# Kernel tuning notes

Hardware: AMD Instinct MI355X
Metric: run time of the kernel (lower is better)

Reference implementation:

```python
import jax, jax.numpy as jnp
import numpy as np


def _dct_last(x):
    """Unnormalized DCT-II along the last axis via the FFT reorder+twiddle trick:
    v[n] = x[2n], v[N-1-n] = x[2n+1];  y[k] = Re( exp(-i*pi*k/(2N)) * FFT(v)[k] )
    => y[k] = sum_n x[n] * cos(pi*(2n+1)*k/(2N))
    This mirrors DREAMPlace's expk (twiddle) formulation.
    """
    N = x.shape[-1]
    v = jnp.concatenate([x[..., ::2], x[..., 1::2][..., ::-1]], axis=-1)
    V = jnp.fft.fft(v)
    k = jnp.arange(N)
    expk = jnp.exp(-1j * jnp.pi * k.astype(x.dtype) / (2.0 * N))
    return jnp.real(V * expk).astype(x.dtype)


def _dct2(x):
    # DCT-II along last axis, then along second-to-last axis (separable 2D DCT).
    y = _dct_last(x)
    y = _dct_last(jnp.swapaxes(y, -1, -2))
    return jnp.swapaxes(y, -1, -2)


def setup_inputs() -> dict:
    key = jax.random.key(0)
    x = jax.random.normal(key, (8, 2048, 2048), dtype=jnp.float32)
    return {"x": x}


def reference(x):
    return _dct2(x)
```

## Files before the change

### kernel.cpp

```cpp
#include <hip/hip_runtime.h>
#include <hip/hip_bf16.h>
#include <hip/hip_fp16.h>


typedef _Float16 half8 __attribute__((ext_vector_type(8)));
typedef float f32x4 __attribute__((ext_vector_type(4)));
typedef unsigned int uint32;

constexpr int BK = 32;
constexpr int BM = 256, BN = 256;
constexpr int KK = 1024;
constexpr int NT = KK / BK;
constexpr int TILE_E = BM * BK;

__device__ __forceinline__ unsigned short f2h_bits(float f) {
  _Float16 h = (_Float16)f;
  return __builtin_bit_cast(unsigned short, h);
}

__device__ __forceinline__ void gload_lds16(const unsigned short* g, unsigned short* l) {
  __builtin_amdgcn_global_load_lds((const __attribute__((address_space(1))) void*)g,
                                   (__attribute__((address_space(3))) void*)l,
                                   16, 0, 0);
}

#define CFENCE asm volatile("" ::: "memory")

__device__ __forceinline__ int swz_idx(int r, int cbyte) {
  int b = (r >> 1) * 128 + ((((r & 1) << 6) | cbyte) ^ (((r >> 1) & 7) << 4));
  return b >> 1;
}

__device__ __forceinline__ void stage_tile(const unsigned short* __restrict__ G,
                                           int rowbase, int k0, int ld,
                                           unsigned short* lds, int wave, int lane) {
#pragma unroll
  for (int c = 0; c < 2; ++c) {
    const int p = c * 64 + wave * 8 + (lane >> 3);
    const int v = (lane & 7) ^ ((lane >> 3) & 7);
    const int r = 2 * p + (v >> 2);
    const int kslot = v & 3;
    const unsigned short* src = G + (size_t)(rowbase + r) * ld + (k0 + kslot * 8);
    unsigned short* dst = lds + (c * 64 + wave * 8) * 64;
    gload_lds16(src, dst);
  }
}

__global__ __launch_bounds__(256) void cvt_fold12(const float* __restrict__ x,
                                                  unsigned short* __restrict__ Xff) {
  int tid = blockIdx.x * 256 + threadIdx.x;
  int m = tid >> 7;
  int b = m >> 10;
  int ui = m & 1023;
  int j0 = (tid & 127) << 3;
  const float* rf = x + ((size_t)b * 2048 + ui) * 2048;
  const float* rb = x + ((size_t)b * 2048 + 2047 - ui) * 2048;
  float4 fa = *(const float4*)(rf + j0);
  float4 fb = *(const float4*)(rf + j0 + 4);
  float4 fc = *(const float4*)(rf + 2040 - j0);
  float4 fd = *(const float4*)(rf + 2044 - j0);
  float4 ga = *(const float4*)(rb + j0);
  float4 gb = *(const float4*)(rb + j0 + 4);
  float4 gc = *(const float4*)(rb + 2040 - j0);
  float4 gd = *(const float4*)(rb + 2044 - j0);
  float f[8] = {fa.x, fa.y, fa.z, fa.w, fb.x, fb.y, fb.z, fb.w};
  float fm[8] = {fd.w, fd.z, fd.y, fd.x, fc.w, fc.z, fc.y, fc.x};
  float g[8] = {ga.x, ga.y, ga.z, ga.w, gb.x, gb.y, gb.z, gb.w};
  float gm[8] = {gd.w, gd.z, gd.y, gd.x, gc.w, gc.z, gc.y, gc.x};
  uint32 ss[4], sd[4], ds[4], dd[4];
#pragma unroll
  for (int e = 0; e < 4; ++e) {
#pragma unroll
    for (int h = 0; h < 2; ++h) {
      int k = 2 * e + h;
      float fs = f[k] + fm[k], fdv = f[k] - fm[k];
      float gs = g[k] + gm[k], gdv = g[k] - gm[k];
      uint32 vss = f2h_bits(fs + gs), vsd = f2h_bits(fdv + gdv);
      uint32 vds = f2h_bits(fs - gs), vdd = f2h_bits(fdv - gdv);
      if (h == 0) { ss[e] = vss; sd[e] = vsd; ds[e] = vds; dd[e] = vdd; }
      else { ss[e] |= vss << 16; sd[e] |= vsd << 16; ds[e] |= vds << 16; dd[e] |= vdd << 16; }
    }
  }
  unsigned short* os = Xff + ((size_t)b * 2048 + ui) * 2048 + j0;
  unsigned short* od = Xff + ((size_t)b * 2048 + 1024 + ui) * 2048 + j0;
  *(uint4*)os = make_uint4(ss[0], ss[1], ss[2], ss[3]);
  *(uint4*)(os + 1024) = make_uint4(sd[0], sd[1], sd[2], sd[3]);
  *(uint4*)od = make_uint4(ds[0], ds[1], ds[2], ds[3]);
  *(uint4*)(od + 1024) = make_uint4(dd[0], dd[1], dd[2], dd[3]);
}

__global__ __launch_bounds__(256) void gen_cos2(unsigned short* __restrict__ Ce,
                                                unsigned short* __restrict__ Co) {
  int idx = blockIdx.x * 256 + threadIdx.x;
  int k = idx >> 10, n = idx & 1023;
  int tn = 2 * n + 1;
  int pe = (tn * (2 * k)) & 8191;
  int po = (tn * (2 * k + 1)) & 8191;
  const float s = 7.6699039394282061e-4f;
  Ce[idx] = f2h_bits(cosf((float)pe * s));
  Co[idx] = f2h_bits(cosf((float)po * s));
}

template <int MODE>
__global__ __launch_bounds__(512) void dct_gemm(
    const unsigned short* __restrict__ Ce, const unsigned short* __restrict__ Co,
    const unsigned short* __restrict__ D, void* __restrict__ outp) {
  __shared__ unsigned short As[4 * TILE_E];
  __shared__ unsigned short Bs[4 * TILE_E];

  const int tid = threadIdx.x;
  const int lane = tid & 63;
  const int wave = tid >> 6;
  const int wr = wave >> 2;
  const int wc = wave & 3;
  const int bm = blockIdx.y * BM;
  const int bn = blockIdx.x * BN;
  const int z = blockIdx.z;

  const unsigned short* Ag;
  const unsigned short* Bg;
  int lda, ldb, arow, brow;
  bool half;
  if (MODE == 0) {
    half = (bn >= 1024);
    Ag = D + (half ? 1024 : 0); lda = 2048; arow = bm;
    Bg = half ? Co : Ce;        ldb = 1024; brow = bn - (half ? 1024 : 0);
  } else {
    half = (bm >= 1024);
    Ag = half ? Co : Ce;        lda = 1024; arow = bm - (half ? 1024 : 0);
    Bg = D + (size_t)z * 4194304u + (half ? 1024 : 0);
    ldb = 2048; brow = bn;
  }

  const int frc = lane & 15;
  const int cb = (lane >> 4) << 4;

  f32x4 acc[8][4] = {};

  stage_tile(Ag, arow, 0, lda, &As[0], wave, lane);
  stage_tile(Bg, brow, 0, ldb, &Bs[0], wave, lane);
  stage_tile(Ag, arow, BK, lda, &As[TILE_E], wave, lane);
  stage_tile(Bg, brow, BK, ldb, &Bs[TILE_E], wave, lane);
  asm volatile("s_waitcnt vmcnt(4)" ::: "memory");
  CFENCE; __builtin_amdgcn_s_barrier(); CFENCE;

  for (int t = 0; t < NT; ++t) {
    const unsigned short* at = &As[(t & 3) * TILE_E];
    const unsigned short* bt = &Bs[(t & 3) * TILE_E];
    half8 af[4], bf[4];

#pragma unroll
    for (int m = 0; m < 4; ++m)
      af[m] = *(const half8*)&at[swz_idx(wr * 128 + m * 16 + frc, cb)];
#pragma unroll
    for (int n = 0; n < 4; ++n)
      bf[n] = *(const half8*)&bt[swz_idx(wc * 64 + n * 16 + frc, cb)];
    if (t + 2 < NT)
      stage_tile(Ag, arow, (t + 2) * BK, lda, &As[((t + 2) & 3) * TILE_E], wave, lane);
    CFENCE; __builtin_amdgcn_s_barrier(); CFENCE;
    __builtin_amdgcn_s_setprio(1);
#pragma unroll
    for (int m = 0; m < 4; ++m)
#pragma unroll
      for (int n = 0; n < 4; ++n)
        acc[m][n] = __builtin_amdgcn_mfma_f32_16x16x32_f16(af[m], bf[n], acc[m][n], 0, 0, 0);
    __builtin_amdgcn_s_setprio(0);

#pragma unroll
    for (int m = 0; m < 4; ++m)
      af[m] = *(const half8*)&at[swz_idx(wr * 128 + 64 + m * 16 + frc, cb)];
    if (t + 2 < NT)
      stage_tile(Bg, brow, (t + 2) * BK, ldb, &Bs[((t + 2) & 3) * TILE_E], wave, lane);
    if (t < NT - 2)
      asm volatile("s_waitcnt vmcnt(4)" ::: "memory");
    else if (t == NT - 2)
      asm volatile("s_waitcnt vmcnt(0)" ::: "memory");
    CFENCE; __builtin_amdgcn_s_barrier(); CFENCE;
    __builtin_amdgcn_s_setprio(1);
#pragma unroll
    for (int m = 0; m < 4; ++m)
#pragma unroll
      for (int n = 0; n < 4; ++n)
        acc[m + 4][n] =
            __builtin_amdgcn_mfma_f32_16x16x32_f16(af[m], bf[n], acc[m + 4][n], 0, 0, 0);
    __builtin_amdgcn_s_setprio(0);
  }

  const int koff = half ? 1024 : 0;
  if (MODE == 0) {
    unsigned short* U2t = (unsigned short*)outp;
#pragma unroll
    for (int mi = 0; mi < 8; ++mi) {
      const int r = bm + wr * 128 + (mi >> 2) * 64 + (mi & 3) * 16 + (lane >> 4) * 4;
      const int b = r >> 11;
      const int rb = r & 2047;
#pragma unroll
      for (int n = 0; n < 4; ++n) {
        const int cpk = bn + wc * 64 + n * 16 + frc;
        const int ktrue = 2 * (cpk - koff) + (half ? 1 : 0);
        uint32 lo = f2h_bits(acc[mi][n][0]) | ((uint32)f2h_bits(acc[mi][n][1]) << 16);
        uint32 hi = f2h_bits(acc[mi][n][2]) | ((uint32)f2h_bits(acc[mi][n][3]) << 16);
        *(uint2*)&U2t[(size_t)b * 4194304 + (size_t)ktrue * 2048 + rb] =
            make_uint2(lo, hi);
      }
    }
  } else {
    float* out = (float*)outp + (size_t)z * 4194304;
#pragma unroll
    for (int mi = 0; mi < 8; ++mi) {
      const int p0 =
          bm + wr * 128 + (mi >> 2) * 64 + (mi & 3) * 16 + (lane >> 4) * 4 - koff;
#pragma unroll
      for (int n = 0; n < 4; ++n) {
        const int cg = bn + wc * 64 + n * 16 + frc;
#pragma unroll
        for (int i = 0; i < 4; ++i) {
          const int rtrue = 2 * (p0 + i) + (half ? 1 : 0);
          out[(size_t)rtrue * 2048 + cg] = acc[mi][n][i];
        }
      }
    }
  }
}

extern "C" void kernel_launch(void* const* d_in, const int* in_sizes, int n_in,
                              void* d_out, int out_size, void* d_ws,
                              size_t ws_size, hipStream_t stream) {
  const float* x = (const float*)d_in[0];
  float* out = (float*)d_out;

  unsigned short* Xff = (unsigned short*)d_ws;
  unsigned short* Ce = Xff + 33554432u;
  unsigned short* Co = Ce + 1048576u;
  unsigned short* U2t = Co + 1048576u;

  cvt_fold12<<<4096, 256, 0, stream>>>(x, Xff);
  gen_cos2<<<4096, 256, 0, stream>>>(Ce, Co);
  dct_gemm<0><<<dim3(8, 64, 1), 512, 0, stream>>>(Ce, Co, Xff, (void*)U2t);
  dct_gemm<1><<<dim3(8, 8, 8), 512, 0, stream>>>(Ce, Co, U2t, (void*)out);
}
```

Measured before the change: 208.5 us.

## Apply second-level even/odd DCT fold to shrink even-index GEMM depth

The even-frequency half of each 1D DCT is folded once more into 4k and 4k+2 classes. A new fused conversion kernel builds four-way butterflies over rows and columns, and a new table generator emits three cosine matrices. Each GEMM stage now runs as two launches: one with K=1024 for the odd outputs and one with K=512 for the two even sub-classes. This cuts total MFMA work by about a quarter. In exchange it adds an extra launch per stage, short K loops whose pipeline prologue and epilogue are proportionally larger, and more complex index mapping in the fold kernel.

Result: no change. 207.0 us (-0.7%).

```diff
diff --git a/kernel.cpp b/kernel.cpp
--- a/kernel.cpp
+++ b/kernel.cpp
@@ -7,11 +7,7 @@
 typedef float f32x4 __attribute__((ext_vector_type(4)));
 typedef unsigned int uint32;
 
-constexpr int BK = 32;
-constexpr int BM = 256, BN = 256;
-constexpr int KK = 1024;
-constexpr int NT = KK / BK;
-constexpr int TILE_E = BM * BK;
+constexpr int TILE_E = 256 * 32;
 
 __device__ __forceinline__ unsigned short f2h_bits(float f) {
   _Float16 h = (_Float16)f;
@@ -46,65 +42,107 @@
   }
 }
 
-__global__ __launch_bounds__(256) void cvt_fold12(const float* __restrict__ x,
+__global__ __launch_bounds__(256) void cvt_fold22(const float* __restrict__ x,
                                                   unsigned short* __restrict__ Xff) {
   int tid = blockIdx.x * 256 + threadIdx.x;
-  int m = tid >> 7;
-  int b = m >> 10;
-  int ui = m & 1023;
-  int j0 = (tid & 127) << 3;
-  const float* rf = x + ((size_t)b * 2048 + ui) * 2048;
-  const float* rb = x + ((size_t)b * 2048 + 2047 - ui) * 2048;
-  float4 fa = *(const float4*)(rf + j0);
-  float4 fb = *(const float4*)(rf + j0 + 4);
-  float4 fc = *(const float4*)(rf + 2040 - j0);
-  float4 fd = *(const float4*)(rf + 2044 - j0);
-  float4 ga = *(const float4*)(rb + j0);
-  float4 gb = *(const float4*)(rb + j0 + 4);
-  float4 gc = *(const float4*)(rb + 2040 - j0);
-  float4 gd = *(const float4*)(rb + 2044 - j0);
-  float f[8] = {fa.x, fa.y, fa.z, fa.w, fb.x, fb.y, fb.z, fb.w};
-  float fm[8] = {fd.w, fd.z, fd.y, fd.x, fc.w, fc.z, fc.y, fc.x};
-  float g[8] = {ga.x, ga.y, ga.z, ga.w, gb.x, gb.y, gb.z, gb.w};
-  float gm[8] = {gd.w, gd.z, gd.y, gd.x, gc.w, gc.z, gc.y, gc.x};
-  uint32 ss[4], sd[4], ds[4], dd[4];
-#pragma unroll
-  for (int e = 0; e < 4; ++e) {
-#pragma unroll
-    for (int h = 0; h < 2; ++h) {
-      int k = 2 * e + h;
-      float fs = f[k] + fm[k], fdv = f[k] - fm[k];
-      float gs = g[k] + gm[k], gdv = g[k] - gm[k];
-      uint32 vss = f2h_bits(fs + gs), vsd = f2h_bits(fdv + gdv);
-      uint32 vds = f2h_bits(fs - gs), vdd = f2h_bits(fdv - gdv);
-      if (h == 0) { ss[e] = vss; sd[e] = vsd; ds[e] = vds; dd[e] = vdd; }
-      else { ss[e] |= vss << 16; sd[e] |= vsd << 16; ds[e] |= vds << 16; dd[e] |= vdd << 16; }
-    }
-  }
-  unsigned short* os = Xff + ((size_t)b * 2048 + ui) * 2048 + j0;
-  unsigned short* od = Xff + ((size_t)b * 2048 + 1024 + ui) * 2048 + j0;
-  *(uint4*)os = make_uint4(ss[0], ss[1], ss[2], ss[3]);
-  *(uint4*)(os + 1024) = make_uint4(sd[0], sd[1], sd[2], sd[3]);
-  *(uint4*)od = make_uint4(ds[0], ds[1], ds[2], ds[3]);
-  *(uint4*)(od + 1024) = make_uint4(dd[0], dd[1], dd[2], dd[3]);
-}
-
-__global__ __launch_bounds__(256) void gen_cos2(unsigned short* __restrict__ Ce,
-                                                unsigned short* __restrict__ Co) {
+  int m = tid >> 6;
+  int b = m >> 9;
+  int v = m & 511;
+  int j0 = (tid & 63) << 3;
+  const float* base = x + (size_t)b * 4194304;
+  const float* rows[4] = {base + (size_t)v * 2048, base + (size_t)(2047 - v) * 2048,
+                          base + (size_t)(1023 - v) * 2048, base + (size_t)(1024 + v) * 2048};
+  unsigned short* o[4] = {
+      Xff + ((size_t)b * 2048 + v) * 2048,
+      Xff + ((size_t)b * 2048 + 512 + v) * 2048,
+      Xff + ((size_t)b * 2048 + 1024 + v) * 2048,
+      Xff + ((size_t)b * 2048 + 2047 - v) * 2048};
+
+#pragma unroll
+  for (int h = 0; h < 2; ++h) {
+    const int ja = j0 + h * 4;
+    const int jb = 1020 - j0 - h * 4;
+    const int jc = 1024 + j0 + h * 4;
+    const int jd = 2044 - j0 - h * 4;
+    float4 va[4], vb[4], vc[4], vd[4];
+#pragma unroll
+    for (int t = 0; t < 4; ++t) {
+      va[t] = *(const float4*)(rows[t] + ja);
+      vb[t] = *(const float4*)(rows[t] + jb);
+      vc[t] = *(const float4*)(rows[t] + jc);
+      vd[t] = *(const float4*)(rows[t] + jd);
+    }
+    unsigned short up[4][4], um[4][4], wn[4][4], wm[4][4];
+#pragma unroll
+    for (int e4 = 0; e4 < 4; ++e4) {
+      float A[4], Bq[4], C[4], Dq[4];
+#pragma unroll
+      for (int t = 0; t < 4; ++t) {
+        A[t] = ((const float*)&va[t])[e4];
+        Bq[t] = ((const float*)&vb[t])[3 - e4];
+        C[t] = ((const float*)&vc[t])[e4];
+        Dq[t] = ((const float*)&vd[t])[3 - e4];
+      }
+      float Av[4] = {A[0] + A[1] + A[2] + A[3], A[0] + A[1] - A[2] - A[3],
+                     A[0] - A[1], A[2] - A[3]};
+      float Bv[4] = {Bq[0] + Bq[1] + Bq[2] + Bq[3], Bq[0] + Bq[1] - Bq[2] - Bq[3],
+                     Bq[0] - Bq[1], Bq[2] - Bq[3]};
+      float Cv[4] = {C[0] + C[1] + C[2] + C[3], C[0] + C[1] - C[2] - C[3],
+                     C[0] - C[1], C[2] - C[3]};
+      float Dv[4] = {Dq[0] + Dq[1] + Dq[2] + Dq[3], Dq[0] + Dq[1] - Dq[2] - Dq[3],
+                     Dq[0] - Dq[1], Dq[2] - Dq[3]};
+#pragma unroll
+      for (int t = 0; t < 4; ++t) {
+        float un = Av[t] + Dv[t];
+        float umr = Bv[t] + Cv[t];
+        up[t][e4] = f2h_bits(un + umr);
+        um[t][e4] = f2h_bits(un - umr);
+        wn[t][e4] = f2h_bits(Av[t] - Dv[t]);
+        wm[t][e4] = f2h_bits(Bv[t] - Cv[t]);
+      }
+    }
+#pragma unroll
+    for (int t = 0; t < 4; ++t) {
+      *(uint2*)(o[t] + ja) =
+          make_uint2(up[t][0] | ((uint32)up[t][1] << 16), up[t][2] | ((uint32)up[t][3] << 16));
+      *(uint2*)(o[t] + 512 + ja) =
+          make_uint2(um[t][0] | ((uint32)um[t][1] << 16), um[t][2] | ((uint32)um[t][3] << 16));
+      *(uint2*)(o[t] + 1024 + ja) =
+          make_uint2(wn[t][0] | ((uint32)wn[t][1] << 16), wn[t][2] | ((uint32)wn[t][3] << 16));
+      *(uint2*)(o[t] + 1024 + jb) =
+          make_uint2(wm[t][3] | ((uint32)wm[t][2] << 16), wm[t][1] | ((uint32)wm[t][0] << 16));
+    }
+  }
+}
+
+__global__ __launch_bounds__(256) void gen_cos3(unsigned short* __restrict__ C4k,
+                                                unsigned short* __restrict__ C2h,
+                                                unsigned short* __restrict__ C4h) {
   int idx = blockIdx.x * 256 + threadIdx.x;
-  int k = idx >> 10, n = idx & 1023;
-  int tn = 2 * n + 1;
-  int pe = (tn * (2 * k)) & 8191;
-  int po = (tn * (2 * k + 1)) & 8191;
   const float s = 7.6699039394282061e-4f;
-  Ce[idx] = f2h_bits(cosf((float)pe * s));
-  Co[idx] = f2h_bits(cosf((float)po * s));
-}
-
-template <int MODE>
+  if (idx < 1048576) {
+    int k = idx >> 10, n = idx & 1023;
+    int t = ((2 * n + 1) * (2 * k + 1)) & 8191;
+    C4k[idx] = f2h_bits(cosf((float)t * s));
+  } else if (idx < 1310720) {
+    int i2 = idx - 1048576;
+    int k = i2 >> 9, n = i2 & 511;
+    int t = ((2 * n + 1) * 4 * k) & 8191;
+    C2h[i2] = f2h_bits(cosf((float)t * s));
+  } else {
+    int i2 = idx - 1310720;
+    int k = i2 >> 9, n = i2 & 511;
+    int t = ((2 * n + 1) * (4 * k + 2)) & 8191;
+    C4h[i2] = f2h_bits(cosf((float)t * s));
+  }
+}
+
+template <int MODE, int SPLIT>
 __global__ __launch_bounds__(512) void dct_gemm(
-    const unsigned short* __restrict__ Ce, const unsigned short* __restrict__ Co,
+    const unsigned short* __restrict__ M0, const unsigned short* __restrict__ M1,
     const unsigned short* __restrict__ D, void* __restrict__ outp) {
+  constexpr int K = SPLIT ? 512 : 1024;
+  constexpr int NT = K / 32;
   __shared__ unsigned short As[4 * TILE_E];
   __shared__ unsigned short Bs[4 * TILE_E];
 
@@ -113,23 +151,29 @@
   const int wave = tid >> 6;
   const int wr = wave >> 2;
   const int wc = wave & 3;
-  const int bm = blockIdx.y * BM;
-  const int bn = blockIdx.x * BN;
+  const int bmx = blockIdx.y;
+  const int bnx = blockIdx.x;
   const int z = blockIdx.z;
 
   const unsigned short* Ag;
   const unsigned short* Bg;
-  int lda, ldb, arow, brow;
-  bool half;
+  int lda, ldb, arow, brow, cls;
   if (MODE == 0) {
-    half = (bn >= 1024);
-    Ag = D + (half ? 1024 : 0); lda = 2048; arow = bm;
-    Bg = half ? Co : Ce;        ldb = 1024; brow = bn - (half ? 1024 : 0);
+    cls = SPLIT ? (bnx >> 1) : 0;
+    Ag = D + (SPLIT ? cls * 512 : 1024);
+    lda = 2048;
+    arow = bmx * 256;
+    Bg = SPLIT ? (cls ? M1 : M0) : M0;
+    ldb = K;
+    brow = (SPLIT ? (bnx & 1) : bnx) * 256;
   } else {
-    half = (bm >= 1024);
-    Ag = half ? Co : Ce;        lda = 1024; arow = bm - (half ? 1024 : 0);
-    Bg = D + (size_t)z * 4194304u + (half ? 1024 : 0);
-    ldb = 2048; brow = bn;
+    cls = SPLIT ? (bmx >> 1) : 0;
+    Ag = SPLIT ? (cls ? M1 : M0) : M0;
+    lda = K;
+    arow = (SPLIT ? (bmx & 1) : bmx) * 256;
+    Bg = D + (size_t)z * 4194304u + (SPLIT ? cls * 512 : 1024);
+    ldb = 2048;
+    brow = bnx * 256;
   }
 
   const int frc = lane & 15;
@@ -139,8 +183,8 @@
 
   stage_tile(Ag, arow, 0, lda, &As[0], wave, lane);
   stage_tile(Bg, brow, 0, ldb, &Bs[0], wave, lane);
-  stage_tile(Ag, arow, BK, lda, &As[TILE_E], wave, lane);
-  stage_tile(Bg, brow, BK, ldb, &Bs[TILE_E], wave, lane);
+  stage_tile(Ag, arow, 32, lda, &As[TILE_E], wave, lane);
+  stage_tile(Bg, brow, 32, ldb, &Bs[TILE_E], wave, lane);
   asm volatile("s_waitcnt vmcnt(4)" ::: "memory");
   CFENCE; __builtin_amdgcn_s_barrier(); CFENCE;
 
@@ -156,7 +200,7 @@
     for (int n = 0; n < 4; ++n)
       bf[n] = *(const half8*)&bt[swz_idx(wc * 64 + n * 16 + frc, cb)];
     if (t + 2 < NT)
-      stage_tile(Ag, arow, (t + 2) * BK, lda, &As[((t + 2) & 3) * TILE_E], wave, lane);
+      stage_tile(Ag, arow, (t + 2) * 32, lda, &As[((t + 2) & 3) * TILE_E], wave, lane);
     CFENCE; __builtin_amdgcn_s_barrier(); CFENCE;
     __builtin_amdgcn_s_setprio(1);
 #pragma unroll
@@ -170,7 +214,7 @@
     for (int m = 0; m < 4; ++m)
       af[m] = *(const half8*)&at[swz_idx(wr * 128 + 64 + m * 16 + frc, cb)];
     if (t + 2 < NT)
-      stage_tile(Bg, brow, (t + 2) * BK, ldb, &Bs[((t + 2) & 3) * TILE_E], wave, lane);
+      stage_tile(Bg, brow, (t + 2) * 32, ldb, &Bs[((t + 2) & 3) * TILE_E], wave, lane);
     if (t < NT - 2)
       asm volatile("s_waitcnt vmcnt(4)" ::: "memory");
     else if (t == NT - 2)
@@ -186,18 +230,17 @@
     __builtin_amdgcn_s_setprio(0);
   }
 
-  const int koff = half ? 1024 : 0;
   if (MODE == 0) {
     unsigned short* U2t = (unsigned short*)outp;
 #pragma unroll
     for (int mi = 0; mi < 8; ++mi) {
-      const int r = bm + wr * 128 + (mi >> 2) * 64 + (mi & 3) * 16 + (lane >> 4) * 4;
+      const int r = arow + wr * 128 + (mi >> 2) * 64 + (mi & 3) * 16 + (lane >> 4) * 4;
       const int b = r >> 11;
       const int rb = r & 2047;
 #pragma unroll
       for (int n = 0; n < 4; ++n) {
-        const int cpk = bn + wc * 64 + n * 16 + frc;
-        const int ktrue = 2 * (cpk - koff) + (half ? 1 : 0);
+        const int ccls = brow + wc * 64 + n * 16 + frc;
+        const int ktrue = SPLIT ? (4 * ccls + 2 * cls) : (2 * ccls + 1);
         uint32 lo = f2h_bits(acc[mi][n][0]) | ((uint32)f2h_bits(acc[mi][n][1]) << 16);
         uint32 hi = f2h_bits(acc[mi][n][2]) | ((uint32)f2h_bits(acc[mi][n][3]) << 16);
         *(uint2*)&U2t[(size_t)b * 4194304 + (size_t)ktrue * 2048 + rb] =
@@ -208,14 +251,13 @@
     float* out = (float*)outp + (size_t)z * 4194304;
 #pragma unroll
     for (int mi = 0; mi < 8; ++mi) {
-      const int p0 =
-          bm + wr * 128 + (mi >> 2) * 64 + (mi & 3) * 16 + (lane >> 4) * 4 - koff;
+      const int p0 = arow + wr * 128 + (mi >> 2) * 64 + (mi & 3) * 16 + (lane >> 4) * 4;
 #pragma unroll
       for (int n = 0; n < 4; ++n) {
-        const int cg = bn + wc * 64 + n * 16 + frc;
+        const int cg = brow + wc * 64 + n * 16 + frc;
 #pragma unroll
         for (int i = 0; i < 4; ++i) {
-          const int rtrue = 2 * (p0 + i) + (half ? 1 : 0);
+          const int rtrue = SPLIT ? (4 * (p0 + i) + 2 * cls) : (2 * (p0 + i) + 1);
           out[(size_t)rtrue * 2048 + cg] = acc[mi][n][i];
         }
       }
@@ -230,12 +272,15 @@
   float* out = (float*)d_out;
 
   unsigned short* Xff = (unsigned short*)d_ws;
-  unsigned short* Ce = Xff + 33554432u;
-  unsigned short* Co = Ce + 1048576u;
-  unsigned short* U2t = Co + 1048576u;
-
-  cvt_fold12<<<4096, 256, 0, stream>>>(x, Xff);
-  gen_cos2<<<4096, 256, 0, stream>>>(Ce, Co);
-  dct_gemm<0><<<dim3(8, 64, 1), 512, 0, stream>>>(Ce, Co, Xff, (void*)U2t);
-  dct_gemm<1><<<dim3(8, 8, 8), 512, 0, stream>>>(Ce, Co, U2t, (void*)out);
-}
+  unsigned short* C4k = Xff + 33554432u;
+  unsigned short* C2h = C4k + 1048576u;
+  unsigned short* C4h = C2h + 262144u;
+  unsigned short* U2t = C4h + 262144u;
+
+  cvt_fold22<<<1024, 256, 0, stream>>>(x, Xff);
+  gen_cos3<<<6144, 256, 0, stream>>>(C4k, C2h, C4h);
+  dct_gemm<0, 0><<<dim3(4, 64, 1), 512, 0, stream>>>(C4k, C4k, Xff, (void*)U2t);
+  dct_gemm<0, 1><<<dim3(4, 64, 1), 512, 0, stream>>>(C2h, C4h, Xff, (void*)U2t);
+  dct_gemm<1, 0><<<dim3(8, 4, 8), 512, 0, stream>>>(C4k, C4k, U2t, (void*)out);
+  dct_gemm<1, 1><<<dim3(8, 4, 8), 512, 0, stream>>>(C2h, C4h, U2t, (void*)out);
+}
```
